# Optimization experiments

Measured on AMD Instinct MI355X. Metric: run time of the kernel, lower is better.

## Reference

```python
import jax, jax.numpy as jnp
import numpy as np
import math

B, S, DM, H, N_HASHES, BUCKET = 1, 1024, 512, 8, 8, 64
HD = DM // H
N_BUCKETS = max(2, 2 * (S // (2 * BUCKET)))   # 16
ROT = max(1, N_BUCKETS // 2)                  # 8


def setup_inputs() -> dict:
    key = jax.random.key(0)
    ks = jax.random.split(key, 6)
    sc = 1.0 / math.sqrt(DM)
    return {
        "x": jax.random.normal(ks[0], (B, S, DM), dtype=jnp.float32),
        "w_qk": (jax.random.normal(ks[1], (DM, DM), dtype=jnp.float32) * sc),
        "b_qk": jnp.zeros((DM,), dtype=jnp.float32),
        "w_v": (jax.random.normal(ks[2], (DM, DM), dtype=jnp.float32) * sc),
        "b_v": jnp.zeros((DM,), dtype=jnp.float32),
        "w_o": (jax.random.normal(ks[3], (DM, DM), dtype=jnp.float32) * sc),
        "b_o": jnp.zeros((DM,), dtype=jnp.float32),
        # random rotations used for LSH hashing (torch.randn in hash_vectors)
        "rotations": jax.random.normal(ks[4], (N_HASHES, H, HD, ROT), dtype=jnp.float32),
    }


def reference(x, w_qk, b_qk, w_v, b_v, w_o, b_o, rotations):
    # projections, split heads: (B, H, S, HD)
    qk = (x @ w_qk + b_qk).reshape(B, S, H, HD).transpose(0, 2, 1, 3)
    v = (x @ w_v + b_v).reshape(B, S, H, HD).transpose(0, 2, 1, 3)

    # LSH bucket assignment: (B, H, S, n_hashes)
    rot = jnp.einsum('bhnd,rhdc->bhnrc', qk, rotations)
    rot = jnp.concatenate([rot, -rot], axis=-1)
    buckets = jnp.argmax(rot, axis=-1)

    # The original gathers (batch, head, pos) jointly per bucket, so attention
    # mixes across batch and head; flatten exactly the same way.
    N = B * H * S
    qkf = qk.reshape(N, HD)
    vf = v.reshape(N, HD)
    bkf = buckets.reshape(N, N_HASHES).T  # (n_hashes, N)

    # dots are shared across hash rounds; only the bucket mask changes
    dots = (qkf @ qkf.T) / math.sqrt(HD)  # (N, N)

    def body(acc, bk):
        same = bk[:, None] == bk[None, :]  # bucket-equality mask
        w = jax.nn.softmax(jnp.where(same, dots, -jnp.inf), axis=-1)
        return acc + w @ vf, None

    out, _ = jax.lax.scan(body, jnp.zeros_like(vf), bkf)
    out = out / N_HASHES

    out = out.reshape(B, H, S, HD).transpose(0, 2, 1, 3).reshape(B, S, DM)
    return out @ w_o + b_o
```

## Files before the change

kernel.cpp:

```cpp
#include <hip/hip_runtime.h>
#include <math.h>

#define S 1024
#define DM 512
#define H 8
#define HD 64
#define NH 8
#define NB 16
#define N 8192
#define SCALE 0.125f
#define EXP2C 0.18033688f

typedef __attribute__((ext_vector_type(4))) float f32x4;
typedef __attribute__((ext_vector_type(8))) short s16x8;
typedef __attribute__((ext_vector_type(4))) short s16x4;

__device__ __forceinline__ short f2bf(float f) {
  union { float f; unsigned u; } a; a.f = f;
  unsigned r = a.u + 0x7fffu + ((a.u >> 16) & 1u);
  return (short)(r >> 16);
}
__device__ __forceinline__ float bf2f(short h) {
  union { unsigned u; float f; } a; a.u = ((unsigned)(unsigned short)h) << 16;
  return a.f;
}
__device__ __forceinline__ int f2bf2(float lo, float hi) {
  return (int)(unsigned short)f2bf(lo) | (((int)f2bf(hi)) << 16);
}

#if __has_builtin(__builtin_amdgcn_mfma_f32_16x16x16_bf16)
#define MFMA_PV(a, b, c) __builtin_amdgcn_mfma_f32_16x16x16_bf16(a, b, c, 0, 0, 0)
#else
#define MFMA_PV(a, b, c) __builtin_amdgcn_mfma_f32_16x16x16bf16_1k(a, b, c, 0, 0, 0)
#endif

__global__ __launch_bounds__(256) void wprep_kernel(
    const float* __restrict__ wqk, const float* __restrict__ wv,
    const float* __restrict__ wo, const float* __restrict__ x,
    short* __restrict__ wtqk, short* __restrict__ wtv, short* __restrict__ wto,
    short* __restrict__ xs, int* __restrict__ cz) {
  int tid = threadIdx.x;
  if (blockIdx.x == 0) cz[tid] = 0;
  if (blockIdx.x >= 192) {
    int xb = blockIdx.x - 192;
    size_t base = ((size_t)xb * 256 + tid) * 16;
    const float4* xp = (const float4*)(x + base);
    float4 f0 = xp[0], f1 = xp[1], f2 = xp[2], f3 = xp[3];
    float vv[16] = {f0.x,f0.y,f0.z,f0.w, f1.x,f1.y,f1.z,f1.w,
                    f2.x,f2.y,f2.z,f2.w, f3.x,f3.y,f3.z,f3.w};
    s16x8 h0[2], h1[2], h2[2];
#pragma unroll
    for (int g = 0; g < 2; ++g)
#pragma unroll
      for (int i = 0; i < 8; ++i) {
        float v = vv[g * 8 + i];
        short a = f2bf(v); float r1 = v - bf2f(a);
        short b = f2bf(r1); short c = f2bf(r1 - bf2f(b));
        h0[g][i] = a; h1[g][i] = b; h2[g][i] = c;
      }
    s16x8* p0 = (s16x8*)(xs + base);
    s16x8* p1 = (s16x8*)(xs + (size_t)S * DM + base);
    s16x8* p2 = (s16x8*)(xs + (size_t)2 * S * DM + base);
    p0[0] = h0[0]; p0[1] = h0[1];
    p1[0] = h1[0]; p1[1] = h1[1];
    p2[0] = h2[0]; p2[1] = h2[1];
    return;
  }
  int mat = blockIdx.x >> 6;
  int tile = blockIdx.x & 63;
  int kt = tile >> 3, dt = tile & 7;
  const float* w = (mat == 0) ? wqk : ((mat == 1) ? wv : wo);

  __shared__ float wlds[64 * 68];
  int kr = tid >> 2, c4 = tid & 3;
  const float4* src = (const float4*)(w + (size_t)(kt * 64 + kr) * DM + dt * 64 + c4 * 16);
#pragma unroll
  for (int i = 0; i < 4; ++i) {
    float4 v = src[i];
    float* d = &wlds[kr * 68 + c4 * 16 + i * 4];
    d[0] = v.x; d[1] = v.y; d[2] = v.z; d[3] = v.w;
  }
  __syncthreads();
  int dr = tid >> 2, kc = tid & 3;
  s16x8 h0a, h0b, h1a, h1b, h2a, h2b;
#pragma unroll
  for (int i = 0; i < 8; ++i) {
    float v = wlds[(kc * 16 + i) * 68 + dr];
    short a = f2bf(v); float r1 = v - bf2f(a);
    short b = f2bf(r1); short c = f2bf(r1 - bf2f(b));
    h0a[i] = a; h1a[i] = b; h2a[i] = c;
  }
#pragma unroll
  for (int i = 0; i < 8; ++i) {
    float v = wlds[(kc * 16 + 8 + i) * 68 + dr];
    short a = f2bf(v); float r1 = v - bf2f(a);
    short b = f2bf(r1); short c = f2bf(r1 - bf2f(b));
    h0b[i] = a; h1b[i] = b; h2b[i] = c;
  }
  size_t dst = (size_t)(dt * 64 + dr) * DM + kt * 64 + kc * 16;
  if (mat == 0) {
    s16x8* p0 = (s16x8*)(wtqk + dst);
    s16x8* p1 = (s16x8*)(wtqk + (size_t)DM * DM + dst);
    s16x8* p2 = (s16x8*)(wtqk + (size_t)2 * DM * DM + dst);
    p0[0] = h0a; p0[1] = h0b; p1[0] = h1a; p1[1] = h1b; p2[0] = h2a; p2[1] = h2b;
  } else if (mat == 1) {
    s16x8* p = (s16x8*)(wtv + dst); p[0] = h0a; p[1] = h0b;
  } else {
    s16x8* p = (s16x8*)(wto + dst); p[0] = h0a; p[1] = h0b;
  }
}

#define PST 72
__global__ __launch_bounds__(256) void projmm_kernel(
    const short* __restrict__ xs, const short* __restrict__ wtqk,
    const short* __restrict__ wtv,
    const float* __restrict__ bqk, const float* __restrict__ bv,
    float* __restrict__ qkpart, short* __restrict__ vb) {
  int mt = blockIdx.x & 15;
  int rest = blockIdx.x >> 4;
  int sp = rest >> 3;
  int head = rest & 7;
  bool isv = (sp == 6);
  int xl = isv ? 0 : ((0x210100 >> (sp << 2)) & 0xF);
  int wl = isv ? 0 : ((0x012010 >> (sp << 2)) & 0xF);
  const short* wt = isv ? wtv : (wtqk + (size_t)wl * DM * DM);
  const short* xsl = xs + (size_t)xl * S * DM;

  __shared__ short a_lds[2][64 * PST];
  __shared__ short b_lds[2][64 * PST];

  int tid = threadIdx.x;
  int wave = tid >> 6, lane = tid & 63;
  int col = lane & 15, quad = lane >> 4;
  int mh = wave & 1, nh2 = wave >> 1;

  f32x4 acc[2][2];
#pragma unroll
  for (int i = 0; i < 2; ++i)
#pragma unroll
    for (int j = 0; j < 2; ++j) acc[i][j] = (f32x4){0.f, 0.f, 0.f, 0.f};

  int sr = tid >> 2, c4 = tid & 3;
  int gran = sr * PST + ((c4 ^ (sr & 3)) << 4);

  {
    const s16x8* xp = (const s16x8*)(xsl + (size_t)(mt * 64 + sr) * DM + c4 * 16);
    s16x8* ad = (s16x8*)&a_lds[0][gran];
    ad[0] = xp[0]; ad[1] = xp[1];
    const s16x8* wp = (const s16x8*)(wt + (size_t)(head * 64 + sr) * DM + c4 * 16);
    s16x8* bd = (s16x8*)&b_lds[0][gran];
    bd[0] = wp[0]; bd[1] = wp[1];
  }
  __syncthreads();

  for (int ci = 0; ci < 8; ++ci) {
    int cur = ci & 1, nxt = cur ^ 1;
    s16x8 px0, px1, pw0, pw1;
    bool has = (ci + 1) < 8;
    if (has) {
      int kc = ci + 1;
      const s16x8* xp = (const s16x8*)(xsl + (size_t)(mt * 64 + sr) * DM + kc * 64 + c4 * 16);
      px0 = xp[0]; px1 = xp[1];
      const s16x8* wp = (const s16x8*)(wt + (size_t)(head * 64 + sr) * DM + kc * 64 + c4 * 16);
      pw0 = wp[0]; pw1 = wp[1];
    }
#pragma unroll
    for (int s2 = 0; s2 < 2; ++s2) {
      s16x8 af[2], bfv[2];
#pragma unroll
      for (int mi = 0; mi < 2; ++mi) {
        int row = mh * 32 + mi * 16 + col;
        int cidx = ((s2 << 1) + (quad >> 1)) ^ (row & 3);
        af[mi] = *(const s16x8*)&a_lds[cur][row * PST + (cidx << 4) + ((quad & 1) << 3)];
      }
#pragma unroll
      for (int ni = 0; ni < 2; ++ni) {
        int row = nh2 * 32 + ni * 16 + col;
        int cidx = ((s2 << 1) + (quad >> 1)) ^ (row & 3);
        bfv[ni] = *(const s16x8*)&b_lds[cur][row * PST + (cidx << 4) + ((quad & 1) << 3)];
      }
#pragma unroll
      for (int mi = 0; mi < 2; ++mi)
#pragma unroll
        for (int ni = 0; ni < 2; ++ni)
          acc[mi][ni] = __builtin_amdgcn_mfma_f32_16x16x32_bf16(af[mi], bfv[ni],
                                                               acc[mi][ni], 0, 0, 0);
    }
    if (has) {
      s16x8* ad = (s16x8*)&a_lds[nxt][gran];
      ad[0] = px0; ad[1] = px1;
      s16x8* bd = (s16x8*)&b_lds[nxt][gran];
      bd[0] = pw0; bd[1] = pw1;
    }
    __syncthreads();
  }
  if (isv) {
#pragma unroll
    for (int ni = 0; ni < 2; ++ni) {
      int nl = nh2 * 32 + ni * 16 + col;
      float bb = bv[head * 64 + nl];
#pragma unroll
      for (int mi = 0; mi < 2; ++mi)
#pragma unroll
        for (int u = 0; u < 4; ++u) {
          int s = mt * 64 + mh * 32 + mi * 16 + quad * 4 + u;
          vb[((size_t)head * S + s) * HD + nl] = f2bf(acc[mi][ni][u] + bb);
        }
    }
  } else {
    float* dst = qkpart + (size_t)sp * N * HD;
#pragma unroll
    for (int ni = 0; ni < 2; ++ni) {
      int nl = nh2 * 32 + ni * 16 + col;
      float bb = (sp == 0) ? bqk[head * 64 + nl] : 0.f;
#pragma unroll
      for (int mi = 0; mi < 2; ++mi)
#pragma unroll
        for (int u = 0; u < 4; ++u) {
          int s = mt * 64 + mh * 32 + mi * 16 + quad * 4 + u;
          dst[((size_t)head * S + s) * HD + nl] = acc[mi][ni][u] + bb;
        }
    }
  }
}

__global__ __launch_bounds__(256) void sumslab_kernel(
    const float* __restrict__ qkpart, float* __restrict__ qkf,
    short* __restrict__ qkb) {
  int idx = blockIdx.x * 256 + threadIdx.x;
  f32x4 s = ((const f32x4*)qkpart)[idx];
#pragma unroll
  for (int sl = 1; sl < 6; ++sl)
    s += ((const f32x4*)(qkpart + (size_t)sl * N * HD))[idx];
  ((f32x4*)qkf)[idx] = s;
  int2 pk = make_int2(f2bf2(s[0], s[1]), f2bf2(s[2], s[3]));
  *(int2*)(qkb + (size_t)idx * 4) = pk;
}

__global__ __launch_bounds__(256) void bucket_kernel(
    const float* __restrict__ qkf, const float* __restrict__ rot,
    int* __restrict__ cursor, int* __restrict__ perm2) {
  __shared__ float Rl[HD * 8];
  __shared__ int lcnt[NB];
  __shared__ int gbase[NB];
  int tid = threadIdx.x;
  int g = blockIdx.x * 256 + tid;
  int n = g & (N - 1);
  int r = g >> 13;
  int h = n >> 10;
  const float* R = rot + (size_t)((r * H + h) * HD) * 8;
  if (tid < 128) ((f32x4*)Rl)[tid] = ((const f32x4*)R)[tid];
  if (tid < NB) lcnt[tid] = 0;

  f32x4 qv[16];
  const f32x4* q4 = (const f32x4*)(qkf + (size_t)n * HD);
#pragma unroll
  for (int d4 = 0; d4 < 16; ++d4) qv[d4] = q4[d4];
  __syncthreads();

  float v[8];
#pragma unroll
  for (int c = 0; c < 8; ++c) v[c] = 0.f;
#pragma unroll
  for (int d4 = 0; d4 < 16; ++d4) {
    f32x4 q = qv[d4];
#pragma unroll
    for (int j = 0; j < 4; ++j) {
      const f32x4* Rr = (const f32x4*)&Rl[(d4 * 4 + j) * 8];
      f32x4 r0 = Rr[0], r1 = Rr[1];
      float qj = q[j];
#pragma unroll
      for (int c = 0; c < 4; ++c) v[c] = fmaf(qj, r0[c], v[c]);
#pragma unroll
      for (int c = 0; c < 4; ++c) v[4 + c] = fmaf(qj, r1[c], v[4 + c]);
    }
  }
  float best = v[0];
  int bi = 0;
#pragma unroll
  for (int c = 1; c < 16; ++c) {
    float val = (c < 8) ? v[c] : -v[c - 8];
    if (val > best) { best = val; bi = c; }
  }

  int lrank = atomicAdd(&lcnt[bi], 1);
  __syncthreads();
  if (tid < NB) gbase[tid] = atomicAdd(&cursor[(r << 4) + tid], lcnt[tid]);
  __syncthreads();
  perm2[(((size_t)(r << 4) + bi) << 13) + gbase[bi] + lrank] = n;
}

#define KT 64
#define KST 72
#define VTS2 72
#define VBUF (64 * VTS2)
__global__ __launch_bounds__(512) void attn_kernel(
    const short* __restrict__ qkb, const short* __restrict__ vb,
    const int* __restrict__ perm2, const int* __restrict__ cursor,
    short* __restrict__ accumB) {
  int bx = blockIdx.x;
  int rb = bx & 127;
  int chunk = bx >> 7;
  int r = rb >> 4;
  int cnt = cursor[rb];
  int q0 = chunk << 7;
  if (q0 >= cnt) return;
  const int* plist = perm2 + ((size_t)rb << 13);

  int tid = threadIdx.x;
  int wave = tid >> 6, lane = tid & 63;
  int col = lane & 15, quad = lane >> 4;

  __shared__ short k_lds[2][KT * KST];
  __shared__ short v_lds[2][VBUF];

  int qslot = q0 + (wave << 4) + col;
  bool qvalid = qslot < cnt;
  int qidx = plist[qvalid ? qslot : 0];
  bool wactive = (q0 + (wave << 4)) < cnt;

  for (int e = tid; e < VBUF; e += 512) ((int*)v_lds)[e] = 0;

  s16x8 qa[2];
#pragma unroll
  for (int s2 = 0; s2 < 2; ++s2)
    qa[s2] = *(const s16x8*)(qkb + (size_t)qidx * HD + s2 * 32 + quad * 8);
  __syncthreads();

  float lsum = 0.f;
  f32x4 o0 = {0,0,0,0}, o1 = {0,0,0,0}, o2 = {0,0,0,0}, o3 = {0,0,0,0};

  int jsk = tid >> 2, csk = tid & 3;
  bool stager = tid < 256;
  int kgran = jsk * KST + ((csk ^ (jsk & 3)) << 4);
  int ksw0 = (jsk + 16 * csk) & 63;
  int ksw1 = (jsk + 16 * csk + 4) & 63;
  int vdr = csk * 16 * VTS2;

  int vrow = col * VTS2;
  int vco = (col >> 3) << 2;

  {
    int nj = min(KT, cnt);
    if (stager && jsk < nj) {
      int gk = plist[jsk];
      const s16x8* kp = (const s16x8*)(qkb + (size_t)gk * HD + (csk << 4));
      const s16x8* vp = (const s16x8*)(vb + (size_t)gk * HD + (csk << 4));
      s16x8 a0 = kp[0], a1 = kp[1], b0 = vp[0], b1 = vp[1];
      s16x8* kd = (s16x8*)&k_lds[0][kgran];
      kd[0] = a0; kd[1] = a1;
      short* vt = &v_lds[0][vdr];
#pragma unroll
      for (int i = 0; i < 8; ++i) {
        vt[i * VTS2 + ksw0] = b0[i];
        vt[(8 + i) * VTS2 + ksw1] = b1[i];
      }
    }
  }
  int pln = 0; bool pln_ok = false;
  if (stager) {
    int i1 = KT + jsk;
    pln_ok = i1 < cnt;
    pln = plist[i1 < 8192 ? i1 : 8191];
  }
  __syncthreads();

  int ntiles = (cnt + KT - 1) >> 6;
  for (int t = 0; t < ntiles; ++t) {
    int jt = t << 6;
    int cur = t & 1, nxt = cur ^ 1;
    s16x8 a0, a1, b0, b1;
    bool pf_ok = stager && pln_ok;
    if (pf_ok) {
      const s16x8* kp = (const s16x8*)(qkb + (size_t)pln * HD + (csk << 4));
      const s16x8* vp = (const s16x8*)(vb + (size_t)pln * HD + (csk << 4));
      a0 = kp[0]; a1 = kp[1]; b0 = vp[0]; b1 = vp[1];
    }
    int pl2 = 0; bool pl2_ok = false;
    if (stager) {
      int i2 = jt + 2 * KT + jsk;
      pl2_ok = i2 < cnt;
      pl2 = plist[i2 < 8192 ? i2 : 8191];
    }
    if (wactive) {
      const short* vtc = v_lds[cur];
      const short* ktc = k_lds[cur];
      f32x4 sA = {0,0,0,0}, sB = {0,0,0,0}, sC = {0,0,0,0}, sD = {0,0,0,0};
#define QK1(C, SA) { int key = ((C) << 4) + col; \
      const short* kb = &ktc[key * KST]; \
      { int cidx = (quad >> 1) ^ (key & 3); \
        s16x8 kf = *(const s16x8*)&kb[(cidx << 4) + ((quad & 1) << 3)]; \
        SA = __builtin_amdgcn_mfma_f32_16x16x32_bf16(kf, qa[0], SA, 0, 0, 0); } \
      { int cidx = (2 + (quad >> 1)) ^ (key & 3); \
        s16x8 kf = *(const s16x8*)&kb[(cidx << 4) + ((quad & 1) << 3)]; \
        SA = __builtin_amdgcn_mfma_f32_16x16x32_bf16(kf, qa[1], SA, 0, 0, 0); } }
      __builtin_amdgcn_s_setprio(1);
      QK1(0, sA) QK1(1, sB) QK1(2, sC) QK1(3, sD)
      __builtin_amdgcn_s_setprio(0);
      s16x4 p0, p1, p2, p3;
#define SM1(C, SA, PF) { int kbase = jt + ((C) << 4) + (quad << 2); \
      float pw[4]; \
      if (kbase + 4 <= cnt) { \
        _Pragma("unroll") for (int u = 0; u < 4; ++u) pw[u] = exp2f(SA[u] * EXP2C); \
      } else { \
        _Pragma("unroll") for (int u = 0; u < 4; ++u) \
          pw[u] = (kbase + u < cnt) ? exp2f(SA[u] * EXP2C) : 0.f; \
      } \
      lsum += (pw[0] + pw[1]) + (pw[2] + pw[3]); \
      int dA_, dB_; \
      asm("v_cvt_pk_bf16_f32 %0, %1, %2" : "=v"(dA_) : "v"(pw[0]), "v"(pw[1])); \
      asm("v_cvt_pk_bf16_f32 %0, %1, %2" : "=v"(dB_) : "v"(pw[2]), "v"(pw[3])); \
      ((int*)&PF)[0] = dA_; ((int*)&PF)[1] = dB_; }
      SM1(0, sA, p0) SM1(1, sB, p1) SM1(2, sC, p2) SM1(3, sD, p3)
#define PV1(C, PF) { int k0s = ((C) << 4) + (quad << 2) + vco; \
      s16x4 va = *(const s16x4*)&vtc[vrow + (k0s & 63)]; \
      s16x4 vb_ = *(const s16x4*)&vtc[16 * VTS2 + vrow + ((k0s + 16) & 63)]; \
      s16x4 vc = *(const s16x4*)&vtc[32 * VTS2 + vrow + ((k0s + 32) & 63)]; \
      s16x4 vd = *(const s16x4*)&vtc[48 * VTS2 + vrow + ((k0s + 48) & 63)]; \
      o0 = MFMA_PV(PF, va, o0); o1 = MFMA_PV(PF, vb_, o1); \
      o2 = MFMA_PV(PF, vc, o2); o3 = MFMA_PV(PF, vd, o3); }
      __builtin_amdgcn_s_setprio(1);
      PV1(0, p0) PV1(1, p1) PV1(2, p2) PV1(3, p3)
      __builtin_amdgcn_s_setprio(0);
#undef QK1
#undef SM1
#undef PV1
    }
    if (pf_ok) {
      s16x8* kd = (s16x8*)&k_lds[nxt][kgran];
      kd[0] = a0; kd[1] = a1;
      short* vt = &v_lds[nxt][vdr];
#pragma unroll
      for (int i = 0; i < 8; ++i) {
        vt[i * VTS2 + ksw0] = b0[i];
        vt[(8 + i) * VTS2 + ksw1] = b1[i];
      }
    }
    pln = pl2; pln_ok = pl2_ok;
    __syncthreads();
  }

  lsum += __shfl_xor(lsum, 16);
  lsum += __shfl_xor(lsum, 32);
  float inv = 1.f / lsum;
#pragma unroll
  for (int u = 0; u < 4; ++u) {
    int slot = (quad << 2) + u;
    int spos = q0 + (wave << 4) + slot;
    float inv_u = __shfl(inv, slot);
    int qidx_u = __shfl(qidx, slot);
    if (spos < cnt) {
      short* dst = accumB + ((size_t)r * N + qidx_u) * HD + col;
      dst[0]  = f2bf(o0[u] * inv_u);
      dst[16] = f2bf(o1[u] * inv_u);
      dst[32] = f2bf(o2[u] * inv_u);
      dst[48] = f2bf(o3[u] * inv_u);
    }
  }
}

__global__ __launch_bounds__(256) void outproj_kernel(
    const short* __restrict__ accumB, const short* __restrict__ wto,
    const float* __restrict__ bo, float* __restrict__ out) {
  int mt = blockIdx.x & 31;
  int nt = blockIdx.x >> 5;
  __shared__ short a_lds[2][32 * PST];
  __shared__ short b_lds[2][64 * PST];
  int tid = threadIdx.x;
  int wave = tid >> 6, lane = tid & 63;
  int col = lane & 15, quad = lane >> 4;
  int mi2 = wave & 1, nh2 = wave >> 1;

  f32x4 acc[2];
  acc[0] = (f32x4){0.f,0.f,0.f,0.f};
  acc[1] = (f32x4){0.f,0.f,0.f,0.f};

  bool isA = tid < 128;
  int sr = tid >> 2, c4 = tid & 3;
  int agran = sr * PST + ((c4 ^ (sr & 3)) << 4);
  int dl = (tid - 128) >> 1, gp = tid & 1;

  {
    if (isA) {
      size_t abase = ((size_t)0 * S + mt * 32 + sr) * HD + c4 * 16;
      float a16[16];
#pragma unroll
      for (int i = 0; i < 16; ++i) a16[i] = 0.f;
#pragma unroll
      for (int r = 0; r < NH; ++r) {
        const short* ap = accumB + (size_t)r * N * HD + abase;
        s16x8 h0 = *(const s16x8*)ap, h1 = *(const s16x8*)(ap + 8);
#pragma unroll
        for (int i = 0; i < 8; ++i) { a16[i] += bf2f(h0[i]); a16[8 + i] += bf2f(h1[i]); }
      }
      s16x8 ha, hb;
#pragma unroll
      for (int i = 0; i < 8; ++i) {
        ha[i] = f2bf(a16[i] * 0.125f); hb[i] = f2bf(a16[8 + i] * 0.125f);
      }
      s16x8* ad = (s16x8*)&a_lds[0][agran];
      ad[0] = ha; ad[1] = hb;
    } else {
      const s16x8* wp = (const s16x8*)(wto + (size_t)(nt * 64 + dl) * DM + gp * 32);
      int g0 = gp * 2;
      s16x8* d0 = (s16x8*)&b_lds[0][dl * PST + ((g0 ^ (dl & 3)) << 4)];
      d0[0] = wp[0]; d0[1] = wp[1];
      s16x8* d1 = (s16x8*)&b_lds[0][dl * PST + (((g0 + 1) ^ (dl & 3)) << 4)];
      d1[0] = wp[2]; d1[1] = wp[3];
    }
  }
  __syncthreads();

  for (int kc = 0; kc < 8; ++kc) {
    int cur = kc & 1, nxt = cur ^ 1;
    bool has = kc + 1 < 8;
    float a16[16];
    s16x8 pb0, pb1, pb2, pb3;
    if (has) {
      if (isA) {
        size_t abase = ((size_t)(kc + 1) * S + mt * 32 + sr) * HD + c4 * 16;
#pragma unroll
        for (int i = 0; i < 16; ++i) a16[i] = 0.f;
#pragma unroll
        for (int r = 0; r < NH; ++r) {
          const short* ap = accumB + (size_t)r * N * HD + abase;
          s16x8 h0 = *(const s16x8*)ap, h1 = *(const s16x8*)(ap + 8);
#pragma unroll
          for (int i = 0; i < 8; ++i) { a16[i] += bf2f(h0[i]); a16[8 + i] += bf2f(h1[i]); }
        }
      } else {
        const s16x8* wp = (const s16x8*)(wto + (size_t)(nt * 64 + dl) * DM +
                                         (kc + 1) * 64 + gp * 32);
        pb0 = wp[0]; pb1 = wp[1]; pb2 = wp[2]; pb3 = wp[3];
      }
    }
#pragma unroll
    for (int s2 = 0; s2 < 2; ++s2) {
      int arow = mi2 * 16 + col;
      int acidx = ((s2 << 1) + (quad >> 1)) ^ (arow & 3);
      s16x8 af = *(const s16x8*)&a_lds[cur][arow * PST + (acidx << 4) + ((quad & 1) << 3)];
      s16x8 bfv[2];
#pragma unroll
      for (int ni = 0; ni < 2; ++ni) {
        int brow = nh2 * 32 + ni * 16 + col;
        int bcidx = ((s2 << 1) + (quad >> 1)) ^ (brow & 3);
        bfv[ni] = *(const s16x8*)&b_lds[cur][brow * PST + (bcidx << 4) + ((quad & 1) << 3)];
      }
#pragma unroll
      for (int ni = 0; ni < 2; ++ni)
        acc[ni] = __builtin_amdgcn_mfma_f32_16x16x32_bf16(af, bfv[ni], acc[ni], 0, 0, 0);
    }
    if (has) {
      if (isA) {
        s16x8 ha, hb;
#pragma unroll
        for (int i = 0; i < 8; ++i) {
          ha[i] = f2bf(a16[i] * 0.125f); hb[i] = f2bf(a16[8 + i] * 0.125f);
        }
        s16x8* ad = (s16x8*)&a_lds[nxt][agran];
        ad[0] = ha; ad[1] = hb;
      } else {
        int g0 = gp * 2;
        s16x8* d0 = (s16x8*)&b_lds[nxt][dl * PST + ((g0 ^ (dl & 3)) << 4)];
        d0[0] = pb0; d0[1] = pb1;
        s16x8* d1 = (s16x8*)&b_lds[nxt][dl * PST + (((g0 + 1) ^ (dl & 3)) << 4)];
        d1[0] = pb2; d1[1] = pb3;
      }
    }
    __syncthreads();
  }
#pragma unroll
  for (int ni = 0; ni < 2; ++ni) {
    int nl = nh2 * 32 + ni * 16 + col;
    int dgl = nt * 64 + nl;
    float bb = bo[dgl];
#pragma unroll
    for (int u = 0; u < 4; ++u) {
      int s = mt * 32 + mi2 * 16 + quad * 4 + u;
      out[(size_t)s * DM + dgl] = acc[ni][u] + bb;
    }
  }
}

extern "C" void kernel_launch(void* const* d_in, const int* in_sizes, int n_in,
                              void* d_out, int out_size, void* d_ws, size_t ws_size,
                              hipStream_t stream) {
  const float* x    = (const float*)d_in[0];
  const float* w_qk = (const float*)d_in[1];
  const float* b_qk = (const float*)d_in[2];
  const float* w_v  = (const float*)d_in[3];
  const float* b_v  = (const float*)d_in[4];
  const float* w_o  = (const float*)d_in[5];
  const float* b_o  = (const float*)d_in[6];
  const float* rot  = (const float*)d_in[7];
  float* out = (float*)d_out;

  char* ws = (char*)d_ws;
  const size_t MB = 1024u * 1024u;
  short* qkb    = (short*)(ws);
  short* vb     = (short*)(ws + 1 * MB);
  float* qkpart = (float*)(ws + 2 * MB);
  short* accumB = (short*)(ws + 2 * MB);
  int* perm2    = (int*)(ws + 10 * MB);
  float* qkf    = (float*)(ws + 18 * MB);
  short* wtqk   = (short*)(ws + 20 * MB);
  short* wtv    = (short*)(ws + 20 * MB + 1536u * 1024);
  short* wto    = (short*)(ws + 22 * MB);
  int* cursor   = (int*)(ws + 22 * MB + 512u * 1024);
  short* xs     = (short*)(ws + 23 * MB);

  wprep_kernel<<<320, 256, 0, stream>>>(w_qk, w_v, w_o, x, wtqk, wtv, wto, xs, cursor);
  projmm_kernel<<<896, 256, 0, stream>>>(xs, wtqk, wtv, b_qk, b_v, qkpart, vb);
  sumslab_kernel<<<512, 256, 0, stream>>>(qkpart, qkf, qkb);
  bucket_kernel<<<(NH * N) / 256, 256, 0, stream>>>(qkf, rot, cursor, perm2);
  attn_kernel<<<64 * 128, 512, 0, stream>>>(qkb, vb, perm2, cursor, accumB);
  outproj_kernel<<<256, 256, 0, stream>>>(accumB, wto, b_o, out);
}
```

Measured before the change: 138.2 us.

## Make attention persistent with an atomic work queue sorted by bucket size

```diff
diff --git a/kernel.cpp b/kernel.cpp
--- a/kernel.cpp
+++ b/kernel.cpp
@@ -290,45 +290,55 @@
   perm2[(((size_t)(r << 4) + bi) << 13) + gbase[bi] + lrank] = n;
 }
 
+__global__ __launch_bounds__(128) void worklist_kernel(
+    int* cursor, int* __restrict__ items) {
+  __shared__ int cnts[128];
+  __shared__ int ord[128];
+  __shared__ int nchs[128];
+  __shared__ int pfx[128];
+  int tid = threadIdx.x;
+  int c = cursor[tid];
+  cnts[tid] = c;
+  __syncthreads();
+  int rank = 0;
+  for (int j = 0; j < 128; ++j) {
+    int cj = cnts[j];
+    rank += (cj > c || (cj == c && j < tid)) ? 1 : 0;
+  }
+  ord[rank] = tid;
+  __syncthreads();
+  int rb = ord[tid];
+  int nch = (cnts[rb] + 127) >> 7;
+  nchs[tid] = nch;
+  __syncthreads();
+  if (tid == 0) {
+    int acc = 0;
+    for (int j = 0; j < 128; ++j) { pfx[j] = acc; acc += nchs[j]; }
+    cursor[132] = acc;
+  }
+  __syncthreads();
+  int base = pfx[tid];
+  for (int k = 0; k < nch; ++k) items[base + k] = (rb << 8) | k;
+}
+
 #define KT 64
 #define KST 72
 #define VTS2 72
 #define VBUF (64 * VTS2)
 __global__ __launch_bounds__(512) void attn_kernel(
     const short* __restrict__ qkb, const short* __restrict__ vb,
-    const int* __restrict__ perm2, const int* __restrict__ cursor,
+    const int* __restrict__ perm2, const int* cursor,
+    const int* __restrict__ items, int* wctr,
     short* __restrict__ accumB) {
-  int bx = blockIdx.x;
-  int rb = bx & 127;
-  int chunk = bx >> 7;
-  int r = rb >> 4;
-  int cnt = cursor[rb];
-  int q0 = chunk << 7;
-  if (q0 >= cnt) return;
-  const int* plist = perm2 + ((size_t)rb << 13);
-
   int tid = threadIdx.x;
   int wave = tid >> 6, lane = tid & 63;
   int col = lane & 15, quad = lane >> 4;
 
   __shared__ short k_lds[2][KT * KST];
   __shared__ short v_lds[2][VBUF];
-
-  int qslot = q0 + (wave << 4) + col;
-  bool qvalid = qslot < cnt;
-  int qidx = plist[qvalid ? qslot : 0];
-  bool wactive = (q0 + (wave << 4)) < cnt;
-
-  for (int e = tid; e < VBUF; e += 512) ((int*)v_lds)[e] = 0;
-
-  s16x8 qa[2];
-#pragma unroll
-  for (int s2 = 0; s2 < 2; ++s2)
-    qa[s2] = *(const s16x8*)(qkb + (size_t)qidx * HD + s2 * 32 + quad * 8);
-  __syncthreads();
-
-  float lsum = 0.f;
-  f32x4 o0 = {0,0,0,0}, o1 = {0,0,0,0}, o2 = {0,0,0,0}, o3 = {0,0,0,0};
+  __shared__ int s_item;
+
+  int nitems = cursor[132];
 
   int jsk = tid >> 2, csk = tid & 3;
   bool stager = tid < 256;
@@ -336,125 +346,152 @@
   int ksw0 = (jsk + 16 * csk) & 63;
   int ksw1 = (jsk + 16 * csk + 4) & 63;
   int vdr = csk * 16 * VTS2;
-
   int vrow = col * VTS2;
   int vco = (col >> 3) << 2;
 
-  {
-    int nj = min(KT, cnt);
-    if (stager && jsk < nj) {
-      int gk = plist[jsk];
-      const s16x8* kp = (const s16x8*)(qkb + (size_t)gk * HD + (csk << 4));
-      const s16x8* vp = (const s16x8*)(vb + (size_t)gk * HD + (csk << 4));
-      s16x8 a0 = kp[0], a1 = kp[1], b0 = vp[0], b1 = vp[1];
-      s16x8* kd = (s16x8*)&k_lds[0][kgran];
-      kd[0] = a0; kd[1] = a1;
-      short* vt = &v_lds[0][vdr];
-#pragma unroll
-      for (int i = 0; i < 8; ++i) {
-        vt[i * VTS2 + ksw0] = b0[i];
-        vt[(8 + i) * VTS2 + ksw1] = b1[i];
-      }
-    }
-  }
-  int pln = 0; bool pln_ok = false;
-  if (stager) {
-    int i1 = KT + jsk;
-    pln_ok = i1 < cnt;
-    pln = plist[i1 < 8192 ? i1 : 8191];
-  }
-  __syncthreads();
-
-  int ntiles = (cnt + KT - 1) >> 6;
-  for (int t = 0; t < ntiles; ++t) {
-    int jt = t << 6;
-    int cur = t & 1, nxt = cur ^ 1;
-    s16x8 a0, a1, b0, b1;
-    bool pf_ok = stager && pln_ok;
-    if (pf_ok) {
-      const s16x8* kp = (const s16x8*)(qkb + (size_t)pln * HD + (csk << 4));
-      const s16x8* vp = (const s16x8*)(vb + (size_t)pln * HD + (csk << 4));
-      a0 = kp[0]; a1 = kp[1]; b0 = vp[0]; b1 = vp[1];
-    }
-    int pl2 = 0; bool pl2_ok = false;
+  for (int e = tid; e < VBUF; e += 512) ((int*)v_lds)[e] = 0;
+
+  while (true) {
+    if (tid == 0) s_item = atomicAdd(wctr, 1);
+    __syncthreads();
+    int item = s_item;
+    if (item >= nitems) break;
+    int enc = items[item];
+    int rb = enc >> 8, chunk = enc & 255;
+    int r = rb >> 4;
+    int cnt = cursor[rb];
+    int q0 = chunk << 7;
+    const int* plist = perm2 + ((size_t)rb << 13);
+
+    int qslot = q0 + (wave << 4) + col;
+    bool qvalid = qslot < cnt;
+    int qidx = plist[qvalid ? qslot : 0];
+    bool wactive = (q0 + (wave << 4)) < cnt;
+
+    s16x8 qa[2];
+#pragma unroll
+    for (int s2 = 0; s2 < 2; ++s2)
+      qa[s2] = *(const s16x8*)(qkb + (size_t)qidx * HD + s2 * 32 + quad * 8);
+
+    float lsum = 0.f;
+    f32x4 o0 = {0,0,0,0}, o1 = {0,0,0,0}, o2 = {0,0,0,0}, o3 = {0,0,0,0};
+
+    {
+      int nj = min(KT, cnt);
+      if (stager && jsk < nj) {
+        int gk = plist[jsk];
+        const s16x8* kp = (const s16x8*)(qkb + (size_t)gk * HD + (csk << 4));
+        const s16x8* vp = (const s16x8*)(vb + (size_t)gk * HD + (csk << 4));
+        s16x8 a0 = kp[0], a1 = kp[1], b0 = vp[0], b1 = vp[1];
+        s16x8* kd = (s16x8*)&k_lds[0][kgran];
+        kd[0] = a0; kd[1] = a1;
+        short* vt = &v_lds[0][vdr];
+#pragma unroll
+        for (int i = 0; i < 8; ++i) {
+          vt[i * VTS2 + ksw0] = b0[i];
+          vt[(8 + i) * VTS2 + ksw1] = b1[i];
+        }
+      }
+    }
+    int pln = 0; bool pln_ok = false;
     if (stager) {
-      int i2 = jt + 2 * KT + jsk;
-      pl2_ok = i2 < cnt;
-      pl2 = plist[i2 < 8192 ? i2 : 8191];
-    }
-    if (wactive) {
-      const short* vtc = v_lds[cur];
-      const short* ktc = k_lds[cur];
-      f32x4 sA = {0,0,0,0}, sB = {0,0,0,0}, sC = {0,0,0,0}, sD = {0,0,0,0};
+      int i1 = KT + jsk;
+      pln_ok = i1 < cnt;
+      pln = plist[i1 < 8192 ? i1 : 8191];
+    }
+    __syncthreads();
+
+    int ntiles = (cnt + KT - 1) >> 6;
+    for (int t = 0; t < ntiles; ++t) {
+      int jt = t << 6;
+      int cur = t & 1, nxt = cur ^ 1;
+      s16x8 a0, a1, b0, b1;
+      bool pf_ok = stager && pln_ok;
+      if (pf_ok) {
+        const s16x8* kp = (const s16x8*)(qkb + (size_t)pln * HD + (csk << 4));
+        const s16x8* vp = (const s16x8*)(vb + (size_t)pln * HD + (csk << 4));
+        a0 = kp[0]; a1 = kp[1]; b0 = vp[0]; b1 = vp[1];
+      }
+      int pl2 = 0; bool pl2_ok = false;
+      if (stager) {
+        int i2 = jt + 2 * KT + jsk;
+        pl2_ok = i2 < cnt;
+        pl2 = plist[i2 < 8192 ? i2 : 8191];
+      }
+      if (wactive) {
+        const short* vtc = v_lds[cur];
+        const short* ktc = k_lds[cur];
+        f32x4 sA = {0,0,0,0}, sB = {0,0,0,0}, sC = {0,0,0,0}, sD = {0,0,0,0};
 #define QK1(C, SA) { int key = ((C) << 4) + col; \
-      const short* kb = &ktc[key * KST]; \
-      { int cidx = (quad >> 1) ^ (key & 3); \
-        s16x8 kf = *(const s16x8*)&kb[(cidx << 4) + ((quad & 1) << 3)]; \
-        SA = __builtin_amdgcn_mfma_f32_16x16x32_bf16(kf, qa[0], SA, 0, 0, 0); } \
-      { int cidx = (2 + (quad >> 1)) ^ (key & 3); \
-        s16x8 kf = *(const s16x8*)&kb[(cidx << 4) + ((quad & 1) << 3)]; \
-        SA = __builtin_amdgcn_mfma_f32_16x16x32_bf16(kf, qa[1], SA, 0, 0, 0); } }
-      __builtin_amdgcn_s_setprio(1);
-      QK1(0, sA) QK1(1, sB) QK1(2, sC) QK1(3, sD)
-      __builtin_amdgcn_s_setprio(0);
-      s16x4 p0, p1, p2, p3;
+        const short* kb = &ktc[key * KST]; \
+        { int cidx = (quad >> 1) ^ (key & 3); \
+          s16x8 kf = *(const s16x8*)&kb[(cidx << 4) + ((quad & 1) << 3)]; \
+          SA = __builtin_amdgcn_mfma_f32_16x16x32_bf16(kf, qa[0], SA, 0, 0, 0); } \
+        { int cidx = (2 + (quad >> 1)) ^ (key & 3); \
+          s16x8 kf = *(const s16x8*)&kb[(cidx << 4) + ((quad & 1) << 3)]; \
+          SA = __builtin_amdgcn_mfma_f32_16x16x32_bf16(kf, qa[1], SA, 0, 0, 0); } }
+        __builtin_amdgcn_s_setprio(1);
+        QK1(0, sA) QK1(1, sB) QK1(2, sC) QK1(3, sD)
+        __builtin_amdgcn_s_setprio(0);
+        s16x4 p0, p1, p2, p3;
 #define SM1(C, SA, PF) { int kbase = jt + ((C) << 4) + (quad << 2); \
-      float pw[4]; \
-      if (kbase + 4 <= cnt) { \
-        _Pragma("unroll") for (int u = 0; u < 4; ++u) pw[u] = exp2f(SA[u] * EXP2C); \
-      } else { \
-        _Pragma("unroll") for (int u = 0; u < 4; ++u) \
-          pw[u] = (kbase + u < cnt) ? exp2f(SA[u] * EXP2C) : 0.f; \
-      } \
-      lsum += (pw[0] + pw[1]) + (pw[2] + pw[3]); \
-      int dA_, dB_; \
-      asm("v_cvt_pk_bf16_f32 %0, %1, %2" : "=v"(dA_) : "v"(pw[0]), "v"(pw[1])); \
-      asm("v_cvt_pk_bf16_f32 %0, %1, %2" : "=v"(dB_) : "v"(pw[2]), "v"(pw[3])); \
-      ((int*)&PF)[0] = dA_; ((int*)&PF)[1] = dB_; }
-      SM1(0, sA, p0) SM1(1, sB, p1) SM1(2, sC, p2) SM1(3, sD, p3)
+        float pw[4]; \
+        if (kbase + 4 <= cnt) { \
+          _Pragma("unroll") for (int u = 0; u < 4; ++u) pw[u] = exp2f(SA[u] * EXP2C); \
+        } else { \
+          _Pragma("unroll") for (int u = 0; u < 4; ++u) \
+            pw[u] = (kbase + u < cnt) ? exp2f(SA[u] * EXP2C) : 0.f; \
+        } \
+        lsum += (pw[0] + pw[1]) + (pw[2] + pw[3]); \
+        int dA_, dB_; \
+        asm("v_cvt_pk_bf16_f32 %0, %1, %2" : "=v"(dA_) : "v"(pw[0]), "v"(pw[1])); \
+        asm("v_cvt_pk_bf16_f32 %0, %1, %2" : "=v"(dB_) : "v"(pw[2]), "v"(pw[3])); \
+        ((int*)&PF)[0] = dA_; ((int*)&PF)[1] = dB_; }
+        SM1(0, sA, p0) SM1(1, sB, p1) SM1(2, sC, p2) SM1(3, sD, p3)
 #define PV1(C, PF) { int k0s = ((C) << 4) + (quad << 2) + vco; \
-      s16x4 va = *(const s16x4*)&vtc[vrow + (k0s & 63)]; \
-      s16x4 vb_ = *(const s16x4*)&vtc[16 * VTS2 + vrow + ((k0s + 16) & 63)]; \
-      s16x4 vc = *(const s16x4*)&vtc[32 * VTS2 + vrow + ((k0s + 32) & 63)]; \
-      s16x4 vd = *(const s16x4*)&vtc[48 * VTS2 + vrow + ((k0s + 48) & 63)]; \
-      o0 = MFMA_PV(PF, va, o0); o1 = MFMA_PV(PF, vb_, o1); \
-      o2 = MFMA_PV(PF, vc, o2); o3 = MFMA_PV(PF, vd, o3); }
-      __builtin_amdgcn_s_setprio(1);
-      PV1(0, p0) PV1(1, p1) PV1(2, p2) PV1(3, p3)
-      __builtin_amdgcn_s_setprio(0);
+        s16x4 va = *(const s16x4*)&vtc[vrow + (k0s & 63)]; \
+        s16x4 vb_ = *(const s16x4*)&vtc[16 * VTS2 + vrow + ((k0s + 16) & 63)]; \
+        s16x4 vc = *(const s16x4*)&vtc[32 * VTS2 + vrow + ((k0s + 32) & 63)]; \
+        s16x4 vd = *(const s16x4*)&vtc[48 * VTS2 + vrow + ((k0s + 48) & 63)]; \
+        o0 = MFMA_PV(PF, va, o0); o1 = MFMA_PV(PF, vb_, o1); \
+        o2 = MFMA_PV(PF, vc, o2); o3 = MFMA_PV(PF, vd, o3); }
+        __builtin_amdgcn_s_setprio(1);
+        PV1(0, p0) PV1(1, p1) PV1(2, p2) PV1(3, p3)
+        __builtin_amdgcn_s_setprio(0);
 #undef QK1
 #undef SM1
 #undef PV1
-    }
-    if (pf_ok) {
-      s16x8* kd = (s16x8*)&k_lds[nxt][kgran];
-      kd[0] = a0; kd[1] = a1;
-      short* vt = &v_lds[nxt][vdr];
-#pragma unroll
-      for (int i = 0; i < 8; ++i) {
-        vt[i * VTS2 + ksw0] = b0[i];
-        vt[(8 + i) * VTS2 + ksw1] = b1[i];
-      }
-    }
-    pln = pl2; pln_ok = pl2_ok;
-    __syncthreads();
-  }
-
-  lsum += __shfl_xor(lsum, 16);
-  lsum += __shfl_xor(lsum, 32);
-  float inv = 1.f / lsum;
-#pragma unroll
-  for (int u = 0; u < 4; ++u) {
-    int slot = (quad << 2) + u;
-    int spos = q0 + (wave << 4) + slot;
-    float inv_u = __shfl(inv, slot);
-    int qidx_u = __shfl(qidx, slot);
-    if (spos < cnt) {
-      short* dst = accumB + ((size_t)r * N + qidx_u) * HD + col;
-      dst[0]  = f2bf(o0[u] * inv_u);
-      dst[16] = f2bf(o1[u] * inv_u);
-      dst[32] = f2bf(o2[u] * inv_u);
-      dst[48] = f2bf(o3[u] * inv_u);
+      }
+      if (pf_ok) {
+        s16x8* kd = (s16x8*)&k_lds[nxt][kgran];
+        kd[0] = a0; kd[1] = a1;
+        short* vt = &v_lds[nxt][vdr];
+#pragma unroll
+        for (int i = 0; i < 8; ++i) {
+          vt[i * VTS2 + ksw0] = b0[i];
+          vt[(8 + i) * VTS2 + ksw1] = b1[i];
+        }
+      }
+      pln = pl2; pln_ok = pl2_ok;
+      __syncthreads();
+    }
+
+    lsum += __shfl_xor(lsum, 16);
+    lsum += __shfl_xor(lsum, 32);
+    float inv = 1.f / lsum;
+#pragma unroll
+    for (int u = 0; u < 4; ++u) {
+      int slot = (quad << 2) + u;
+      int spos = q0 + (wave << 4) + slot;
+      float inv_u = __shfl(inv, slot);
+      int qidx_u = __shfl(qidx, slot);
+      if (spos < cnt) {
+        short* dst = accumB + ((size_t)r * N + qidx_u) * HD + col;
+        dst[0]  = f2bf(o0[u] * inv_u);
+        dst[16] = f2bf(o1[u] * inv_u);
+        dst[32] = f2bf(o2[u] * inv_u);
+        dst[48] = f2bf(o3[u] * inv_u);
+      }
     }
   }
 }
@@ -608,11 +645,14 @@
   short* wto    = (short*)(ws + 22 * MB);
   int* cursor   = (int*)(ws + 22 * MB + 512u * 1024);
   short* xs     = (short*)(ws + 23 * MB);
+  int* items    = (int*)(ws + 26 * MB);
 
   wprep_kernel<<<320, 256, 0, stream>>>(w_qk, w_v, w_o, x, wtqk, wtv, wto, xs, cursor);
   projmm_kernel<<<896, 256, 0, stream>>>(xs, wtqk, wtv, b_qk, b_v, qkpart, vb);
   sumslab_kernel<<<512, 256, 0, stream>>>(qkpart, qkf, qkb);
   bucket_kernel<<<(NH * N) / 256, 256, 0, stream>>>(qkf, rot, cursor, perm2);
-  attn_kernel<<<64 * 128, 512, 0, stream>>>(qkb, vb, perm2, cursor, accumB);
+  worklist_kernel<<<1, 128, 0, stream>>>(cursor, items);
+  attn_kernel<<<768, 512, 0, stream>>>(qkb, vb, perm2, cursor, items,
+                                       cursor + 128, accumB);
   outproj_kernel<<<256, 256, 0, stream>>>(accumB, wto, b_o, out);
 }
```

New measurement: 152.1 us. +10.1%, slower.
